# Kernel tuning notes

Measured on AMD Instinct MI355X. Metric: run time of the kernel, lower is better.

Reference implementation:

```python
import jax, jax.numpy as jnp
import numpy as np

B, Q, K = 4, 1024, 2048
QDIM, MDIM, EDIM, H = 1024, 1024, 1024, 16
HD = EDIM // H

def setup_inputs() -> dict:
    key = jax.random.key(0)
    ks = jax.random.split(key, 7)
    s = lambda d: (1.0 / np.sqrt(d))
    return {
        'query': jax.random.normal(ks[0], (B, Q, QDIM), jnp.float32),
        'memory': jax.random.normal(ks[1], (B, K, MDIM), jnp.float32),
        'bias': jax.random.normal(ks[2], (B, K), jnp.float32),
        'Wq': jax.random.normal(ks[3], (QDIM, EDIM), jnp.float32) * s(QDIM),
        'Wk': jax.random.normal(ks[4], (MDIM, EDIM), jnp.float32) * s(MDIM),
        'Wv': jax.random.normal(ks[5], (MDIM, EDIM), jnp.float32) * s(MDIM),
        'Wo': jax.random.normal(ks[6], (EDIM, EDIM), jnp.float32) * s(EDIM),
    }

def reference(query, memory, bias, Wq, Wk, Wv, Wo):
    scale = HD ** -0.5
    # projections -> [B, H, Q/K, HD]
    q = (query @ Wq).reshape(B, Q, H, HD).transpose(0, 2, 1, 3)
    k = (memory @ Wk).reshape(B, K, H, HD).transpose(0, 2, 1, 3)
    v = (memory @ Wv).reshape(B, K, H, HD).transpose(0, 2, 1, 3)
    scores = jnp.einsum('bhqd,bhkd->bhqk', q, k) * scale
    scores = scores + bias[:, None, None, :]
    weights = jax.nn.softmax(scores, axis=-1)
    out = jnp.einsum('bhqk,bhkd->bhqd', weights, v)
    out = out.transpose(0, 2, 1, 3).reshape(B, Q, EDIM)
    return out @ Wo
```

## Files before the change

kernel.cpp:

```cpp
#include <hip/hip_runtime.h>
#include <cstdint>
#include <cstddef>

typedef unsigned short u16;
typedef __attribute__((ext_vector_type(8))) short bf16x8;
typedef __attribute__((ext_vector_type(4))) short bf16x4;
typedef __attribute__((ext_vector_type(4))) float f32x4;
typedef __attribute__((ext_vector_type(16))) float f32x16;

#define B_  4
#define Q_  1024
#define K_  2048
#define E_  1024
#define H_  16
#define HD_ 64
#define LOG2E 1.4426950408889634f
#define M0_  16.0f

__device__ inline u16 f2bf(float f) {
  union { float f; uint32_t u; } x; x.f = f;
  return (u16)((x.u + 0x7fffu + ((x.u >> 16) & 1u)) >> 16);
}

__device__ inline short bfc(float f) {
  __bf16 h = (__bf16)f;
  return __builtin_bit_cast(short, h);
}

__device__ inline void gload16(const u16* g, void* l) {
  __builtin_amdgcn_global_load_lds((const __attribute__((address_space(1))) void*)g,
                                   (__attribute__((address_space(3))) void*)l, 16, 0, 0);
}

#define NQ8 (B_ * Q_ * E_ / 8)
#define NM8 (B_ * K_ * E_ / 8)
#define NBI (B_ * K_)
#define NPREP ((NQ8 + NM8 + NBI) / 256)
__global__ __launch_bounds__(256) void prep_all(const float* __restrict__ query,
                                                const float* __restrict__ memory,
                                                const float* __restrict__ bias,
                                                const float* W0, const float* W1,
                                                const float* W2, const float* W3,
                                                u16* __restrict__ qb,
                                                u16* __restrict__ mb,
                                                float* __restrict__ bias2,
                                                u16* T0, u16* T1, u16* T2, u16* T3) {
  __shared__ float t[64][65];
  int bid = blockIdx.x;
  if (bid < NPREP) {
    int i = bid * 256 + threadIdx.x;
    const float* src;
    u16* dst;
    if (i < NQ8) {
      src = query + (size_t)i * 8; dst = qb + (size_t)i * 8;
    } else if (i < NQ8 + NM8) {
      int j = i - NQ8;
      src = memory + (size_t)j * 8; dst = mb + (size_t)j * 8;
    } else {
      int j = i - (NQ8 + NM8);
      if (j < NBI) bias2[j] = bias[j] * LOG2E - M0_;
      return;
    }
    float4 a = *reinterpret_cast<const float4*>(src);
    float4 b = *reinterpret_cast<const float4*>(src + 4);
    union { u16 u[8]; uint4 v; } r;
    r.u[0] = f2bf(a.x); r.u[1] = f2bf(a.y); r.u[2] = f2bf(a.z); r.u[3] = f2bf(a.w);
    r.u[4] = f2bf(b.x); r.u[5] = f2bf(b.y); r.u[6] = f2bf(b.z); r.u[7] = f2bf(b.w);
    *reinterpret_cast<uint4*>(dst) = r.v;
  } else {
    int tb = bid - NPREP;
    int z = tb >> 8, xy = tb & 255;
    const float* W; u16* T;
    switch (z) {
      case 0: W = W0; T = T0; break;
      case 1: W = W1; T = T1; break;
      case 2: W = W2; T = T2; break;
      default: W = W3; T = T3; break;
    }
    int k0 = (xy & 15) * 64, n0 = (xy >> 4) * 64;
    int r = threadIdx.x >> 6, c = threadIdx.x & 63;
#pragma unroll
    for (int i = 0; i < 16; ++i)
      t[r + i * 4][c] = W[(size_t)(k0 + r + i * 4) * E_ + n0 + c];
    __syncthreads();
#pragma unroll
    for (int i = 0; i < 16; ++i)
      T[(size_t)(n0 + r + i * 4) * E_ + k0 + c] = f2bf(t[c][r + i * 4]);
  }
}

template <int MODE>
__device__ __forceinline__ void gemm_body(const u16* __restrict__ A,
                                          const u16* __restrict__ Bt,
                                          void* __restrict__ C,
                                          int M, int N, int Kc, int bx, int by,
                                          char* lds) {
  const int tid = threadIdx.x;
  const int w = tid >> 6, l = tid & 63;
  const int wr = w >> 1, wc = w & 1;
  const int lr = l & 15, lg = l >> 4;
  const int m0 = bx * 128, n0 = by * 128;

  const int e0g = tid * 8, e1g = e0g + 2048;
  const int row0 = e0g >> 5, row1 = e1g >> 5;
  const int lc0 = ((((e0g & 31) >> 3) ^ ((row0 >> 1) & 3)) * 8);
  const int lc1 = ((((e1g & 31) >> 3) ^ ((row1 >> 1) & 3)) * 8);
  const u16* Ar0 = A  + (size_t)(m0 + row0) * Kc + lc0;
  const u16* Ar1 = A  + (size_t)(m0 + row1) * Kc + lc1;
  const u16* Br0 = Bt + (size_t)(n0 + row0) * Kc + lc0;
  const u16* Br1 = Bt + (size_t)(n0 + row1) * Kc + lc1;
  const int d0 = tid * 16, d1 = d0 + 4096;

  const int ck = (lg ^ ((lr >> 1) & 3)) * 16;
  int aofs = (wr * 64 + lr) * 64 + ck;
  int bofs = 16384 + (wc * 64 + lr) * 64 + ck;

  f32x4 acc[4][4];
#pragma unroll
  for (int mt = 0; mt < 4; ++mt)
#pragma unroll
    for (int nt = 0; nt < 4; ++nt)
      acc[mt][nt] = (f32x4){0.f, 0.f, 0.f, 0.f};

  gload16(Ar0, lds + d0);
  gload16(Ar1, lds + d1);
  gload16(Br0, lds + 16384 + d0);
  gload16(Br1, lds + 16384 + d1);
  __syncthreads();

  const int NI = Kc >> 5;
  for (int ki = 0; ki < NI; ++ki) {
    if (ki + 1 < NI) {
      const int nb = ((ki & 1) ^ 1) * 8192;
      const int kk = (ki + 1) * 32;
      gload16(Ar0 + kk, lds + nb + d0);
      gload16(Ar1 + kk, lds + nb + d1);
      gload16(Br0 + kk, lds + 16384 + nb + d0);
      gload16(Br1 + kk, lds + 16384 + nb + d1);
    }

    bf16x8 a[4], b[4];
#pragma unroll
    for (int mt = 0; mt < 4; ++mt)
      a[mt] = *reinterpret_cast<const bf16x8*>(lds + aofs + mt * 1024);
#pragma unroll
    for (int nt = 0; nt < 4; ++nt)
      b[nt] = *reinterpret_cast<const bf16x8*>(lds + bofs + nt * 1024);
    __builtin_amdgcn_s_setprio(1);
#pragma unroll
    for (int mt = 0; mt < 4; ++mt)
#pragma unroll
      for (int nt = 0; nt < 4; ++nt)
        acc[mt][nt] = __builtin_amdgcn_mfma_f32_16x16x32_bf16(a[mt], b[nt], acc[mt][nt], 0, 0, 0);
    __builtin_amdgcn_s_setprio(0);

    aofs ^= 8192; bofs ^= 8192;
    __syncthreads();
  }

#pragma unroll
  for (int mt = 0; mt < 4; ++mt) {
#pragma unroll
    for (int nt = 0; nt < 4; ++nt) {
      int col = n0 + wc * 64 + nt * 16 + lr;
#pragma unroll
      for (int j = 0; j < 4; ++j) {
        int row = m0 + wr * 64 + mt * 16 + lg * 4 + j;
        float v = acc[mt][nt][j];
        if (MODE == 1) {
          ((u16*)C)[(size_t)row * N + col] = f2bf(v);
        } else if (MODE == 3) {
          ((u16*)C)[(size_t)row * N + col] = f2bf(v * (0.125f * LOG2E));
        } else {
          ((u16*)C)[((size_t)((col >> 11) * 16 + (row >> 6)) * 64 + (row & 63)) * 2048 + (col & 2047)] = f2bf(v);
        }
      }
    }
  }
}

__global__ __launch_bounds__(512) void gemm_out(const u16* __restrict__ A,
                                                const u16* __restrict__ Bt,
                                                float* __restrict__ C,
                                                int N, int Kc) {
  __shared__ uint4 lds4[2048];
  char* lds = (char*)lds4;
  int d = blockIdx.x;
  int bid = (d & 7) * 32 + (d >> 3);
  const int bx = bid >> 3, by = bid & 7;
  const int tid = threadIdx.x;
  const int w = tid >> 6, l = tid & 63;
  const int wrow = w >> 2, wcol = w & 3;
  const int lr = l & 15, lg = l >> 4;
  const int m0 = bx * 128, n0 = by * 128;

  const int e = tid * 8;
  const int row = e >> 5;
  const int lc = ((((e & 31) >> 3) ^ ((row >> 1) & 3)) * 8);
  const u16* Ar = A  + (size_t)(m0 + row) * Kc + lc;
  const u16* Br = Bt + (size_t)(n0 + row) * Kc + lc;
  const int dd = tid * 16;

  const int ck = (lg ^ ((lr >> 1) & 3)) * 16;
  int aofs = (wrow * 64 + lr) * 64 + ck;
  int bofs = 16384 + (wcol * 32 + lr) * 64 + ck;

  f32x4 acc[4][2];
#pragma unroll
  for (int mt = 0; mt < 4; ++mt)
#pragma unroll
    for (int nt = 0; nt < 2; ++nt)
      acc[mt][nt] = (f32x4){0.f, 0.f, 0.f, 0.f};

  gload16(Ar, lds + dd);
  gload16(Br, lds + 16384 + dd);
  __syncthreads();

  const int NI = Kc >> 5;
  for (int ki = 0; ki < NI; ++ki) {
    if (ki + 1 < NI) {
      const int nb = ((ki & 1) ^ 1) * 8192;
      const int kk = (ki + 1) * 32;
      gload16(Ar + kk, lds + nb + dd);
      gload16(Br + kk, lds + 16384 + nb + dd);
    }

    bf16x8 a[4], b[2];
#pragma unroll
    for (int mt = 0; mt < 4; ++mt)
      a[mt] = *reinterpret_cast<const bf16x8*>(lds + aofs + mt * 1024);
#pragma unroll
    for (int nt = 0; nt < 2; ++nt)
      b[nt] = *reinterpret_cast<const bf16x8*>(lds + bofs + nt * 1024);
    __builtin_amdgcn_s_setprio(1);
#pragma unroll
    for (int mt = 0; mt < 4; ++mt)
#pragma unroll
      for (int nt = 0; nt < 2; ++nt)
        acc[mt][nt] = __builtin_amdgcn_mfma_f32_16x16x32_bf16(a[mt], b[nt], acc[mt][nt], 0, 0, 0);
    __builtin_amdgcn_s_setprio(0);

    aofs ^= 8192; bofs ^= 8192;
    __syncthreads();
  }

#pragma unroll
  for (int mt = 0; mt < 4; ++mt) {
#pragma unroll
    for (int nt = 0; nt < 2; ++nt) {
      int col = n0 + wcol * 32 + nt * 16 + lr;
#pragma unroll
      for (int j = 0; j < 4; ++j) {
        int rowc = m0 + wrow * 64 + mt * 16 + lg * 4 + j;
        C[(size_t)rowc * N + col] = acc[mt][nt][j];
      }
    }
  }
}

__global__ __launch_bounds__(256) void proj_fused(const u16* __restrict__ qb,
                                                  const u16* __restrict__ mb,
                                                  const u16* __restrict__ wqt,
                                                  const u16* __restrict__ wkt,
                                                  const u16* __restrict__ wvt,
                                                  u16* __restrict__ qproj,
                                                  u16* __restrict__ kproj,
                                                  u16* __restrict__ vt) {
  __shared__ uint4 lds4[2048];
  char* lds = (char*)lds4;
  int d = blockIdx.x;
  int bid = (d & 7) * 160 + (d >> 3);
  if (bid < 256) {
    gemm_body<3>(qb, wqt, qproj, B_ * Q_, E_, E_, bid >> 3, bid & 7, lds);
  } else if (bid < 768) {
    int i = bid - 256;
    gemm_body<1>(mb, wkt, kproj, B_ * K_, E_, E_, i >> 3, i & 7, lds);
  } else {
    int i = bid - 768;
    gemm_body<2>(wvt, mb, vt, E_, B_ * K_, E_, i & 7, i >> 3, lds);
  }
}

__global__ __launch_bounds__(256, 4) void attn_kernel(const u16* __restrict__ qp,
                                                      const u16* __restrict__ kp,
                                                      const u16* __restrict__ vT,
                                                      const float* __restrict__ bias2,
                                                      u16* __restrict__ out) {
  __shared__ uint4 lds4[2048];
  char* ldsb = (char*)lds4;

  const int blk = blockIdx.x;
  const int hg = blk & 63, qt = blk >> 6;
  const int b = hg >> 4, h = hg & 15;
  const int tid = threadIdx.x;
  const int w = tid >> 6, l = tid & 63;
  const int wq = w & 1, wk = w >> 1;
  const int l31 = l & 31, lh = l >> 5;

  const int bk4 = l31 >> 2;
  const int t4 = bk4 & 3;
  const int pk31 = (((t4 == 1) || (t4 == 2)) ? (bk4 ^ 3) : bk4) * 4 + (l31 & 3);

  bf16x8 qf[4];
  const u16* qrow = qp + (size_t)(b * Q_ + qt * 64 + wq * 32 + l31) * E_ + h * 64 + lh * 8;
#pragma unroll
  for (int st = 0; st < 4; ++st)
    qf[st] = *reinterpret_cast<const bf16x8*>(qrow + st * 16);

  f32x16 O0, O1;
#pragma unroll
  for (int i = 0; i < 16; ++i) { O0[i] = 0.f; O1[i] = 0.f; }
  float OsumL = 0.f;

  const float* bias_b = bias2 + (size_t)b * K_;
  const u16* kbase = kp + (size_t)b * K_ * E_ + h * 64;
  const u16* vbase = vT + (size_t)(b * H_ + h) * HD_ * K_;

  const int xkk = (pk31 & 7) * 8;
  const int xvv = (l31 & 7) * 8;
  int kofs[4];
#pragma unroll
  for (int st = 0; st < 4; ++st)
    kofs[st] = (wk * 32 + pk31) * 128 + (((st * 16 + lh * 8) ^ xkk) << 1);
  int vofs[2];
#pragma unroll
  for (int ksl = 0; ksl < 2; ++ksl)
    vofs[ksl] = 16384 + l31 * 128 + (((wk * 32 + ksl * 16 + lh * 8) ^ xvv) << 1);

  const float* btp = bias_b + wk * 32 + lh * 8;
  float4 bg0 = *reinterpret_cast<const float4*>(btp);
  float4 bg1 = *reinterpret_cast<const float4*>(btp + 4);
  float4 bg2 = *reinterpret_cast<const float4*>(btp + 16);
  float4 bg3 = *reinterpret_cast<const float4*>(btp + 20);

  const int e0 = tid * 8, e1 = e0 + 2048;
  const int r0 = e0 >> 6, r1 = e1 >> 6;
  const int sc0 = (e0 & 63) ^ ((r0 & 7) * 8);
  const int sc1 = (e1 & 63) ^ ((r1 & 7) * 8);
  const u16* kp0 = kbase + (size_t)r0 * E_ + sc0;
  const u16* kp1 = kbase + (size_t)r1 * E_ + sc1;
  const u16* vp0 = vbase + (size_t)r0 * K_ + sc0;
  const u16* vp1 = vbase + (size_t)r1 * K_ + sc1;

  gload16(kp0, ldsb + tid * 16);
  gload16(kp1, ldsb + 4096 + tid * 16);
  gload16(vp0, ldsb + 16384 + tid * 16);
  gload16(vp1, ldsb + 16384 + 4096 + tid * 16);
  __syncthreads();

  const int NT = K_ / 64;
  for (int t = 0; t < NT; ++t) {
    if (t + 1 < NT) {
      const int nb = ((t & 1) ^ 1) * 8192;
      kp0 += (size_t)64 * E_; kp1 += (size_t)64 * E_;
      vp0 += 64; vp1 += 64;
      gload16(kp0, ldsb + nb + tid * 16);
      gload16(kp1, ldsb + nb + 4096 + tid * 16);
      gload16(vp0, ldsb + 16384 + nb + tid * 16);
      gload16(vp1, ldsb + 16384 + nb + 4096 + tid * 16);
    }

    f32x16 S;
    S[0] = bg0.x; S[1] = bg0.y; S[2] = bg0.z; S[3] = bg0.w;
    S[4] = bg1.x; S[5] = bg1.y; S[6] = bg1.z; S[7] = bg1.w;
    S[8] = bg2.x; S[9] = bg2.y; S[10] = bg2.z; S[11] = bg2.w;
    S[12] = bg3.x; S[13] = bg3.y; S[14] = bg3.z; S[15] = bg3.w;

    float4 ng0 = bg0, ng1 = bg1, ng2 = bg2, ng3 = bg3;
    if (t + 1 < NT) {
      btp += 64;
      ng0 = *reinterpret_cast<const float4*>(btp);
      ng1 = *reinterpret_cast<const float4*>(btp + 4);
      ng2 = *reinterpret_cast<const float4*>(btp + 16);
      ng3 = *reinterpret_cast<const float4*>(btp + 20);
    }

    __builtin_amdgcn_s_setprio(1);
#pragma unroll
    for (int st = 0; st < 4; ++st) {
      bf16x8 ka = *reinterpret_cast<const bf16x8*>(ldsb + kofs[st]);
      S = __builtin_amdgcn_mfma_f32_32x32x16_bf16(ka, qf[st], S, 0, 0, 0);
    }
    __builtin_amdgcn_s_setprio(0);

#pragma unroll
    for (int i = 0; i < 16; ++i) S[i] = __builtin_amdgcn_exp2f(S[i]);
    float ps = ((S[0] + S[1]) + (S[2] + S[3])) + ((S[4] + S[5]) + (S[6] + S[7]))
             + ((S[8] + S[9]) + (S[10] + S[11])) + ((S[12] + S[13]) + (S[14] + S[15]));
    OsumL += ps;

    uint32_t u[8];
#pragma unroll
    for (int j = 0; j < 8; ++j) {
      float plo = S[2 * j], phi = S[2 * j + 1];
      asm("v_cvt_pk_bf16_f32 %0, %1, %2" : "=v"(u[j]) : "v"(plo), "v"(phi));
    }
    bf16x8 P0 = __builtin_bit_cast(bf16x8, (uint4){u[0], u[1], u[2], u[3]});
    bf16x8 P1 = __builtin_bit_cast(bf16x8, (uint4){u[4], u[5], u[6], u[7]});

    __builtin_amdgcn_s_setprio(1);
    {
      bf16x8 va;
      va = *reinterpret_cast<const bf16x8*>(ldsb + vofs[0]);
      O0 = __builtin_amdgcn_mfma_f32_32x32x16_bf16(va, P0, O0, 0, 0, 0);
      va = *reinterpret_cast<const bf16x8*>(ldsb + vofs[0] + 4096);
      O1 = __builtin_amdgcn_mfma_f32_32x32x16_bf16(va, P0, O1, 0, 0, 0);
      va = *reinterpret_cast<const bf16x8*>(ldsb + vofs[1]);
      O0 = __builtin_amdgcn_mfma_f32_32x32x16_bf16(va, P1, O0, 0, 0, 0);
      va = *reinterpret_cast<const bf16x8*>(ldsb + vofs[1] + 4096);
      O1 = __builtin_amdgcn_mfma_f32_32x32x16_bf16(va, P1, O1, 0, 0, 0);
    }
    __builtin_amdgcn_s_setprio(0);

    bg0 = ng0; bg1 = ng1; bg2 = ng2; bg3 = ng3;
    kofs[0] ^= 8192; kofs[1] ^= 8192; kofs[2] ^= 8192; kofs[3] ^= 8192;
    vofs[0] ^= 8192; vofs[1] ^= 8192;
    __syncthreads();
  }

  float Osum = OsumL + __shfl_xor(OsumL, 32, 64);

  float* ex = (float*)ldsb + (size_t)(wq * 64 + l) * 33;
  if (wk == 1) {
#pragma unroll
    for (int i = 0; i < 16; ++i) ex[i] = O0[i];
#pragma unroll
    for (int i = 0; i < 16; ++i) ex[16 + i] = O1[i];
    ex[32] = Osum;
  }
  __syncthreads();
  if (wk == 0) {
#pragma unroll
    for (int i = 0; i < 16; ++i) O0[i] += ex[i];
#pragma unroll
    for (int i = 0; i < 16; ++i) O1[i] += ex[16 + i];
    Osum += ex[32];
    float inv = 1.f / Osum;
    u16* orow = out + (size_t)(b * Q_ + qt * 64 + wq * 32 + l31) * E_ + h * 64;
#pragma unroll
    for (int g = 0; g < 4; ++g) {
      int hd0 = 8 * g + 4 * lh;
#pragma unroll
      for (int j = 0; j < 4; ++j) {
        orow[hd0 + j] = (u16)bfc(O0[4 * g + j] * inv);
        orow[32 + hd0 + j] = (u16)bfc(O1[4 * g + j] * inv);
      }
    }
  }
}

extern "C" void kernel_launch(void* const* d_in, const int* in_sizes, int n_in,
                              void* d_out, int out_size, void* d_ws, size_t ws_size,
                              hipStream_t stream) {
  const float* query  = (const float*)d_in[0];
  const float* memory = (const float*)d_in[1];
  const float* bias   = (const float*)d_in[2];
  const float* Wq     = (const float*)d_in[3];
  const float* Wk     = (const float*)d_in[4];
  const float* Wv     = (const float*)d_in[5];
  const float* Wo     = (const float*)d_in[6];
  float* out = (float*)d_out;

  char* p = (char*)d_ws;
  u16* qb    = (u16*)p; p += (size_t)B_ * Q_ * E_ * 2;
  u16* mb    = (u16*)p; p += (size_t)B_ * K_ * E_ * 2;
  u16* wqt   = (u16*)p; p += (size_t)E_ * E_ * 2;
  u16* wkt   = (u16*)p; p += (size_t)E_ * E_ * 2;
  u16* wvt   = (u16*)p; p += (size_t)E_ * E_ * 2;
  u16* wot   = (u16*)p; p += (size_t)E_ * E_ * 2;
  u16* qproj = (u16*)p; p += (size_t)B_ * Q_ * E_ * 2;
  u16* kproj = (u16*)p; p += (size_t)B_ * K_ * E_ * 2;
  u16* vt    = (u16*)p; p += (size_t)B_ * K_ * E_ * 2;
  u16* attn  = (u16*)p; p += (size_t)B_ * Q_ * E_ * 2;
  float* bias2 = (float*)p; p += (size_t)B_ * K_ * 4;

  prep_all<<<NPREP + 1024, 256, 0, stream>>>(query, memory, bias, Wq, Wk, Wv, Wo,
                                             qb, mb, bias2, wqt, wkt, wvt, wot);

  proj_fused<<<1280, 256, 0, stream>>>(qb, mb, wqt, wkt, wvt, qproj, kproj, vt);

  attn_kernel<<<B_ * H_ * (Q_ / 64), 256, 0, stream>>>(qproj, kproj, vt, bias2, attn);

  gemm_out<<<256, 512, 0, stream>>>(attn, wot, out, E_, E_);
}
```

Measured before the change: 135.9 us.

## Triple-buffer LDS in projection and output GEMMs with prefetch distance two

```diff
diff --git a/kernel.cpp b/kernel.cpp
--- a/kernel.cpp
+++ b/kernel.cpp
@@ -112,8 +112,8 @@
   const int d0 = tid * 16, d1 = d0 + 4096;
 
   const int ck = (lg ^ ((lr >> 1) & 3)) * 16;
-  int aofs = (wr * 64 + lr) * 64 + ck;
-  int bofs = 16384 + (wc * 64 + lr) * 64 + ck;
+  const int aofs = (wr * 64 + lr) * 64 + ck;
+  const int bofs = (wc * 64 + lr) * 64 + ck;
 
   f32x4 acc[4][4];
 #pragma unroll
@@ -124,28 +124,33 @@
 
   gload16(Ar0, lds + d0);
   gload16(Ar1, lds + d1);
-  gload16(Br0, lds + 16384 + d0);
-  gload16(Br1, lds + 16384 + d1);
-  __syncthreads();
+  gload16(Br0, lds + 24576 + d0);
+  gload16(Br1, lds + 24576 + d1);
+  gload16(Ar0 + 32, lds + 8192 + d0);
+  gload16(Ar1 + 32, lds + 8192 + d1);
+  gload16(Br0 + 32, lds + 24576 + 8192 + d0);
+  gload16(Br1 + 32, lds + 24576 + 8192 + d1);
+  asm volatile("s_waitcnt vmcnt(4)" ::: "memory");
+  __builtin_amdgcn_s_barrier();
 
   const int NI = Kc >> 5;
+  int rb = 0, wb = 16384;
   for (int ki = 0; ki < NI; ++ki) {
-    if (ki + 1 < NI) {
-      const int nb = ((ki & 1) ^ 1) * 8192;
-      const int kk = (ki + 1) * 32;
-      gload16(Ar0 + kk, lds + nb + d0);
-      gload16(Ar1 + kk, lds + nb + d1);
-      gload16(Br0 + kk, lds + 16384 + nb + d0);
-      gload16(Br1 + kk, lds + 16384 + nb + d1);
+    if (ki + 2 < NI) {
+      const int kk = (ki + 2) * 32;
+      gload16(Ar0 + kk, lds + wb + d0);
+      gload16(Ar1 + kk, lds + wb + d1);
+      gload16(Br0 + kk, lds + 24576 + wb + d0);
+      gload16(Br1 + kk, lds + 24576 + wb + d1);
     }
 
     bf16x8 a[4], b[4];
 #pragma unroll
     for (int mt = 0; mt < 4; ++mt)
-      a[mt] = *reinterpret_cast<const bf16x8*>(lds + aofs + mt * 1024);
+      a[mt] = *reinterpret_cast<const bf16x8*>(lds + rb + aofs + mt * 1024);
 #pragma unroll
     for (int nt = 0; nt < 4; ++nt)
-      b[nt] = *reinterpret_cast<const bf16x8*>(lds + bofs + nt * 1024);
+      b[nt] = *reinterpret_cast<const bf16x8*>(lds + 24576 + rb + bofs + nt * 1024);
     __builtin_amdgcn_s_setprio(1);
 #pragma unroll
     for (int mt = 0; mt < 4; ++mt)
@@ -154,8 +159,14 @@
         acc[mt][nt] = __builtin_amdgcn_mfma_f32_16x16x32_bf16(a[mt], b[nt], acc[mt][nt], 0, 0, 0);
     __builtin_amdgcn_s_setprio(0);
 
-    aofs ^= 8192; bofs ^= 8192;
-    __syncthreads();
+    if (ki + 2 < NI) {
+      asm volatile("s_waitcnt vmcnt(4)" ::: "memory");
+    } else {
+      asm volatile("s_waitcnt vmcnt(0)" ::: "memory");
+    }
+    __builtin_amdgcn_s_barrier();
+    rb = (rb == 16384) ? 0 : rb + 8192;
+    wb = (wb == 16384) ? 0 : wb + 8192;
   }
 
 #pragma unroll
@@ -183,7 +194,7 @@
                                                 const u16* __restrict__ Bt,
                                                 float* __restrict__ C,
                                                 int N, int Kc) {
-  __shared__ uint4 lds4[2048];
+  __shared__ uint4 lds4[3072];
   char* lds = (char*)lds4;
   int d = blockIdx.x;
   int bid = (d & 7) * 32 + (d >> 3);
@@ -202,8 +213,8 @@
   const int dd = tid * 16;
 
   const int ck = (lg ^ ((lr >> 1) & 3)) * 16;
-  int aofs = (wrow * 64 + lr) * 64 + ck;
-  int bofs = 16384 + (wcol * 32 + lr) * 64 + ck;
+  const int aofs = (wrow * 64 + lr) * 64 + ck;
+  const int bofs = (wcol * 32 + lr) * 64 + ck;
 
   f32x4 acc[4][2];
 #pragma unroll
@@ -213,25 +224,28 @@
       acc[mt][nt] = (f32x4){0.f, 0.f, 0.f, 0.f};
 
   gload16(Ar, lds + dd);
-  gload16(Br, lds + 16384 + dd);
-  __syncthreads();
+  gload16(Br, lds + 24576 + dd);
+  gload16(Ar + 32, lds + 8192 + dd);
+  gload16(Br + 32, lds + 24576 + 8192 + dd);
+  asm volatile("s_waitcnt vmcnt(2)" ::: "memory");
+  __builtin_amdgcn_s_barrier();
 
   const int NI = Kc >> 5;
+  int rb = 0, wb = 16384;
   for (int ki = 0; ki < NI; ++ki) {
-    if (ki + 1 < NI) {
-      const int nb = ((ki & 1) ^ 1) * 8192;
-      const int kk = (ki + 1) * 32;
-      gload16(Ar + kk, lds + nb + dd);
-      gload16(Br + kk, lds + 16384 + nb + dd);
+    if (ki + 2 < NI) {
+      const int kk = (ki + 2) * 32;
+      gload16(Ar + kk, lds + wb + dd);
+      gload16(Br + kk, lds + 24576 + wb + dd);
     }
 
     bf16x8 a[4], b[2];
 #pragma unroll
     for (int mt = 0; mt < 4; ++mt)
-      a[mt] = *reinterpret_cast<const bf16x8*>(lds + aofs + mt * 1024);
+      a[mt] = *reinterpret_cast<const bf16x8*>(lds + rb + aofs + mt * 1024);
 #pragma unroll
     for (int nt = 0; nt < 2; ++nt)
-      b[nt] = *reinterpret_cast<const bf16x8*>(lds + bofs + nt * 1024);
+      b[nt] = *reinterpret_cast<const bf16x8*>(lds + 24576 + rb + bofs + nt * 1024);
     __builtin_amdgcn_s_setprio(1);
 #pragma unroll
     for (int mt = 0; mt < 4; ++mt)
@@ -240,8 +254,14 @@
         acc[mt][nt] = __builtin_amdgcn_mfma_f32_16x16x32_bf16(a[mt], b[nt], acc[mt][nt], 0, 0, 0);
     __builtin_amdgcn_s_setprio(0);
 
-    aofs ^= 8192; bofs ^= 8192;
-    __syncthreads();
+    if (ki + 2 < NI) {
+      asm volatile("s_waitcnt vmcnt(2)" ::: "memory");
+    } else {
+      asm volatile("s_waitcnt vmcnt(0)" ::: "memory");
+    }
+    __builtin_amdgcn_s_barrier();
+    rb = (rb == 16384) ? 0 : rb + 8192;
+    wb = (wb == 16384) ? 0 : wb + 8192;
   }
 
 #pragma unroll
@@ -266,7 +286,7 @@
                                                   u16* __restrict__ qproj,
                                                   u16* __restrict__ kproj,
                                                   u16* __restrict__ vt) {
-  __shared__ uint4 lds4[2048];
+  __shared__ uint4 lds4[3072];
   char* lds = (char*)lds4;
   int d = blockIdx.x;
   int bid = (d & 7) * 160 + (d >> 3);
```

Measured after the change: 134.9 us, median of 2. No clear change (-0.8%).
